# Kernel optimization log

Measured on AMD Instinct MI355X. Metric: run time of the kernel, lower is better.

Reference implementation:

```python
import jax, jax.numpy as jnp
import numpy as np

N, IN, OUT, H = 8192, 128, 64, 4
NEG_SLOPE = 0.2   # GATConv leaky-relu slope
EPS = 1e-5        # BatchNorm1d eps
MASK_VAL = -1e9   # masked_fill value for non-edges (finite for grad safety)


def setup_inputs() -> dict:
    key = jax.random.key(0)
    ks = jax.random.split(key, 5)
    x = jax.random.normal(ks[0], (N, IN), jnp.float32)
    adj = jax.random.randint(ks[1], (N, N), 0, 2, jnp.int32)  # dense 0/1 adjacency
    W = jax.random.normal(ks[2], (H, IN, OUT), jnp.float32) * (1.0 / np.sqrt(IN))
    a_i = jax.random.normal(ks[3], (H, OUT), jnp.float32) * (1.0 / np.sqrt(OUT))
    a_j = jax.random.normal(ks[4], (H, OUT), jnp.float32) * (1.0 / np.sqrt(OUT))
    gamma = jnp.ones((H * OUT,), jnp.float32)   # BN weight
    beta = jnp.zeros((H * OUT,), jnp.float32)   # BN bias
    return {"x": x, "adj": adj, "W": W, "a_i": a_i, "a_j": a_j,
            "gamma": gamma, "beta": beta}


def reference(x, adj, W, a_i, a_j, gamma, beta):
    # --- GATConv (dense adjacency, multi-head, concat) ---
    h = jnp.einsum('ni,hio->hno', x, W)              # [H, N, OUT]
    ei = jnp.einsum('hno,ho->hn', h, a_i)            # [H, N] source scores
    ej = jnp.einsum('hno,ho->hn', h, a_j)            # [H, N] target scores
    coe = ei[:, :, None] + ej[:, None, :]            # [H, N, N]
    coe = jnp.where(coe >= 0, coe, NEG_SLOPE * coe)  # leaky_relu
    coe = jnp.where(adj[None, :, :] == 0, MASK_VAL, coe)
    att = jax.nn.softmax(coe, axis=-1)               # segment softmax over neighbors
    out = jnp.einsum('hnm,hmo->hno', att, h)         # weighted aggregation
    out = jnp.transpose(out, (1, 0, 2)).reshape(N, H * OUT)  # concat heads
    # --- BatchNorm1d (training-mode batch stats over nodes) ---
    mean = jnp.mean(out, axis=0)
    var = jnp.var(out, axis=0)
    out = (out - mean) * jax.lax.rsqrt(var + EPS) * gamma + beta
    # --- ReLU ---
    return jax.nn.relu(out)
```

## Files before the change

kernel.cpp:

```cpp
#include <hip/hip_runtime.h>
#include <hip/hip_bf16.h>

#define NN   8192
#define IND  128
#define OUTD 64
#define NH   4
#define NEG_SLOPE 0.2f
#define BN_EPS 1e-5f

typedef __attribute__((ext_vector_type(8))) short     bf16x8;
typedef __attribute__((ext_vector_type(8))) _Float16  f16x8;
typedef __attribute__((ext_vector_type(2))) _Float16  h2;
typedef __attribute__((ext_vector_type(4))) float     f32x4;
typedef __attribute__((ext_vector_type(4))) int       i32x4;

union V4 { i32x4 i; f16x8 v; };

static __device__ __forceinline__ short f2bf(float f) {
    union { float f; unsigned u; } v; v.f = f;
    return (short)((v.u + 0x8000u) >> 16);
}
static __device__ __forceinline__ unsigned short f2h(float f) {
    union { _Float16 h; unsigned short s; } u; u.h = (_Float16)f; return u.s;
}

__global__ __launch_bounds__(256) void k0_repackW(const float* __restrict__ W,
                                                  short* __restrict__ WB) {
    int tid = blockIdx.x * 256 + threadIdx.x;
    int o = tid & 63, i = (tid >> 6) & 127, h = tid >> 13;
    WB[((h * 16 + (i >> 3)) * 64 + o) * 8 + (i & 7)] = f2bf(W[(h * 128 + i) * 64 + o]);
}

__global__ __launch_bounds__(256) void k1_feat(const float* __restrict__ x,
                                               const short* __restrict__ WB,
                                               const float* __restrict__ a_i,
                                               const float* __restrict__ a_j,
                                               unsigned short* __restrict__ hF,
                                               float* __restrict__ t_Ri,
                                               unsigned short* __restrict__ tE1,
                                               unsigned short* __restrict__ tE2) {
    int w = threadIdx.x >> 6;
    int l = threadIdx.x & 63;
    int quad = l >> 4, lx = l & 15;
    int rb = blockIdx.x;

    f32x4 acc[4] = {};
#pragma unroll
    for (int ks = 0; ks < 4; ++ks) {
        const float* xp = x + (rb * 16 + lx) * IND + ks * 32 + quad * 8;
        f32x4 xa = *(const f32x4*)xp;
        f32x4 xb = *(const f32x4*)(xp + 4);
        bf16x8 af;
#pragma unroll
        for (int j = 0; j < 4; ++j) { af[j] = f2bf(xa[j]); af[4 + j] = f2bf(xb[j]); }
#pragma unroll
        for (int ot = 0; ot < 4; ++ot) {
            bf16x8 bf = *(const bf16x8*)(WB + ((w * 16 + ks * 4 + quad) * 64 + ot * 16 + lx) * 8);
            acc[ot] = __builtin_amdgcn_mfma_f32_16x16x32_bf16(af, bf, acc[ot], 0, 0, 0);
        }
    }
    float aiv[4], ajv[4];
#pragma unroll
    for (int ot = 0; ot < 4; ++ot) {
        aiv[ot] = a_i[w * 64 + ot * 16 + lx];
        ajv[ot] = a_j[w * 64 + ot * 16 + lx];
    }
#pragma unroll
    for (int reg = 0; reg < 4; ++reg) {
        int row = rb * 16 + quad * 4 + reg;
        float ei = 0.f, ej = 0.f;
#pragma unroll
        for (int ot = 0; ot < 4; ++ot) {
            float hv = acc[ot][reg];
            ei += hv * aiv[ot];
            ej += hv * ajv[ot];
        }
#pragma unroll
        for (int m = 1; m <= 8; m <<= 1) {
            ei += __shfl_xor(ei, m, 64);
            ej += __shfl_xor(ej, m, 64);
        }
        if (lx == reg) {
            t_Ri[w * NN + row] = expf(-0.8f * ei);
            tE1[w * NN + row] = f2h(expf(ej));
            tE2[w * NN + row] = f2h(expf(NEG_SLOPE * ej));
        }
#pragma unroll
        for (int ot = 0; ot < 4; ++ot) {
            int o = ot * 16 + lx;
            hF[((w * 1024 + (row >> 3)) * 64 + o) * 8 + (row & 7)] = f2h(acc[ot][reg]);
        }
    }
}

__global__ __launch_bounds__(256) void k2_attn(const int* __restrict__ adj,
                                               const unsigned short* __restrict__ hF,
                                               const float* __restrict__ t_Ri,
                                               const unsigned short* __restrict__ tE1,
                                               const unsigned short* __restrict__ tE2,
                                               float* __restrict__ num,
                                               float* __restrict__ Lsum) {
    __shared__ unsigned char smask[128 * 68];
    __shared__ unsigned int  lutm[256 * 4];
    int tid = threadIdx.x;
    int w = tid >> 6;
    int l = tid & 63;
    int quad = l >> 4, lx = l & 15;
    int rb = blockIdx.x & 127, ks = blockIdx.x >> 7;
    int rowbase = rb * 64;
    int tb = w * NN;
    int k0 = ks * 1024;

    {
        unsigned b = (unsigned)tid;
        i32x4 e;
#pragma unroll
        for (int jj = 0; jj < 4; ++jj) {
            unsigned lo = (b >> (2 * jj)) & 1u, hi = (b >> (2 * jj + 1)) & 1u;
            e[jj] = (int)(lo * 0x3C00u + hi * 0x3C000000u);
        }
        *(i32x4*)&lutm[tid * 4] = e;
    }

    {
        int cg = tid & 127, half = tid >> 7;
        const int* abase = adj + (size_t)rowbase * NN + k0 + cg * 8;
#pragma unroll 2
        for (int rr = 0; rr < 8; ++rr) {
            int rl = half * 8 + rr;
            unsigned mword = 0;
#pragma unroll
            for (int rh = 0; rh < 4; ++rh) {
                const int* ap = abase + (size_t)(rh * 16 + rl) * NN;
                i32x4 a0 = *(const i32x4*)ap;
                i32x4 a1 = *(const i32x4*)(ap + 4);
                unsigned m = 0;
#pragma unroll
                for (int j = 0; j < 4; ++j) {
                    m |= (a0[j] ? 1u : 0u) << j;
                    m |= (a1[j] ? 1u : 0u) << (4 + j);
                }
                mword |= m << (8 * rh);
            }
            *(unsigned int*)&smask[cg * 68 + rl * 4] = mword;
        }
    }
    __syncthreads();

    h2 Rh2[4];
#pragma unroll
    for (int r = 0; r < 4; ++r) {
        _Float16 rv = (_Float16)t_Ri[tb + rowbase + r * 16 + lx];
        Rh2[r][0] = rv; Rh2[r][1] = rv;
    }

    V4 ones;
#pragma unroll
    for (int jj = 0; jj < 4; ++jj) ones.i[jj] = 0x3C003C00;

    f32x4 acc[4][4] = {};
    f32x4 accL[4] = {};

    i32x4 p1, p2;
    V4 pbf[4];
    unsigned pm32;
    {
        int kb = k0 + quad * 8;
        p1 = *(const i32x4*)(tE1 + tb + kb);
        p2 = *(const i32x4*)(tE2 + tb + kb);
#pragma unroll
        for (int ot = 0; ot < 4; ++ot)
            pbf[ot].i = *(const i32x4*)(hF + ((w * 1024 + (kb >> 3)) * 64 + ot * 16 + lx) * 8);
        pm32 = *(const unsigned int*)&smask[quad * 68 + lx * 4];
    }

#pragma unroll 2
    for (int kt = 0; kt < 32; ++kt) {
        i32x4 t1 = p1, t2 = p2;
        unsigned m32 = pm32;
        V4 bfrag[4];
#pragma unroll
        for (int ot = 0; ot < 4; ++ot) bfrag[ot] = pbf[ot];

        int ktn = (kt + 1) & 31;
        int kbn = k0 + ktn * 32 + quad * 8;
        p1 = *(const i32x4*)(tE1 + tb + kbn);
        p2 = *(const i32x4*)(tE2 + tb + kbn);
#pragma unroll
        for (int ot = 0; ot < 4; ++ot)
            pbf[ot].i = *(const i32x4*)(hF + ((w * 1024 + (kbn >> 3)) * 64 + ot * 16 + lx) * 8);
        pm32 = *(const unsigned int*)&smask[(ktn * 4 + quad) * 68 + lx * 4];

        V4 afr[4];
#pragma unroll
        for (int r = 0; r < 4; ++r) {
            V4 mw;
            mw.i = *(const i32x4*)&lutm[((m32 >> (8 * r)) & 0xFFu) * 4];
#pragma unroll
            for (int jj = 0; jj < 4; ++jj) {
                h2 e1 = __builtin_bit_cast(h2, (unsigned)t1[jj]);
                h2 e2 = __builtin_bit_cast(h2, (unsigned)t2[jj]);
                h2 mk = __builtin_bit_cast(h2, (unsigned)mw.i[jj]);
                h2 p  = __builtin_elementwise_max(e1, Rh2[r] * e2) * mk;
                afr[r].i[jj] = (int)__builtin_bit_cast(unsigned, p);
            }
        }
#pragma unroll
        for (int r = 0; r < 4; ++r)
            accL[r] = __builtin_amdgcn_mfma_f32_16x16x32_f16(afr[r].v, ones.v, accL[r], 0, 0, 0);
#pragma unroll
        for (int r = 0; r < 4; ++r)
#pragma unroll
            for (int ot = 0; ot < 4; ++ot)
                acc[r][ot] = __builtin_amdgcn_mfma_f32_16x16x32_f16(afr[r].v, bfrag[ot].v, acc[r][ot], 0, 0, 0);
    }

#pragma unroll
    for (int r = 0; r < 4; ++r)
        if (lx == 0)
#pragma unroll
            for (int reg = 0; reg < 4; ++reg)
                atomicAdd(&Lsum[w * NN + rowbase + r * 16 + quad * 4 + reg], accL[r][reg]);
#pragma unroll
    for (int r = 0; r < 4; ++r)
#pragma unroll
        for (int ot = 0; ot < 4; ++ot)
#pragma unroll
            for (int reg = 0; reg < 4; ++reg) {
                int row = rowbase + r * 16 + quad * 4 + reg;
                atomicAdd(&num[row * 256 + w * 64 + ot * 16 + lx], acc[r][ot][reg]);
            }
}

__global__ __launch_bounds__(256) void k3_stats(const float* __restrict__ num,
                                                const float* __restrict__ Lsum,
                                                float* __restrict__ stats) {
    int c = threadIdx.x;
    int h = c >> 6;
    float s = 0.f, s2 = 0.f;
#pragma unroll
    for (int rr = 0; rr < 8; ++rr) {
        int row = blockIdx.x * 8 + rr;
        float val = num[row * 256 + c] / Lsum[h * NN + row];
        s += val; s2 += val * val;
    }
    atomicAdd(&stats[c], s);
    atomicAdd(&stats[c + 256], s2);
}

__global__ __launch_bounds__(256) void k5_apply(const float* __restrict__ num,
                                                const float* __restrict__ Lsum,
                                                const float* __restrict__ stats,
                                                const float* __restrict__ gamma,
                                                const float* __restrict__ beta,
                                                float* __restrict__ out) {
    __shared__ float sbnp[512];
    int c = threadIdx.x;
    float mean = stats[c] * (1.0f / NN);
    float var  = stats[c + 256] * (1.0f / NN) - mean * mean;
    float sc = gamma[c] * rsqrtf(var + BN_EPS);
    sbnp[c] = sc;
    sbnp[c + 256] = beta[c] - mean * sc;
    __syncthreads();

    int g = blockIdx.x * 256 + threadIdx.x;
    f32x4 v = *(const f32x4*)(num + (size_t)g * 4);
    int cb = (g * 4) & 255;
    int row = g >> 6;
    float rL = 1.0f / Lsum[(cb >> 6) * NN + row];
    f32x4 r;
#pragma unroll
    for (int j = 0; j < 4; ++j)
        r[j] = fmaxf((v[j] * rL) * sbnp[cb + j] + sbnp[256 + cb + j], 0.0f);
    *(f32x4*)(out + (size_t)g * 4) = r;
}

extern "C" void kernel_launch(void* const* d_in, const int* in_sizes, int n_in,
                              void* d_out, int out_size, void* d_ws, size_t ws_size,
                              hipStream_t stream) {
    (void)in_sizes; (void)n_in; (void)out_size; (void)ws_size;
    const float* x     = (const float*)d_in[0];
    const int*   adj   = (const int*)d_in[1];
    const float* W     = (const float*)d_in[2];
    const float* a_i   = (const float*)d_in[3];
    const float* a_j   = (const float*)d_in[4];
    const float* gamma = (const float*)d_in[5];
    const float* beta  = (const float*)d_in[6];
    float* out = (float*)d_out;

    char* ws = (char*)d_ws;
    short*          WB    = (short*)(ws + 0);
    unsigned short* hF    = (unsigned short*)(ws + 65536);
    float*          t_Ri  = (float*)(ws + 4259840);
    unsigned short* tE1   = (unsigned short*)(ws + 4390912);
    unsigned short* tE2   = (unsigned short*)(ws + 4456448);
    float*          num   = (float*)(ws + 4521984);
    float*          Lsum  = (float*)(ws + 12910592);
    float*          stats = (float*)(ws + 13041664);

    (void)hipMemsetAsync(num, 0, 8388608 + 131072 + 2048, stream);

    k0_repackW<<<dim3(128),  dim3(256), 0, stream>>>(W, WB);
    k1_feat   <<<dim3(512),  dim3(256), 0, stream>>>(x, WB, a_i, a_j, hF, t_Ri, tE1, tE2);
    k2_attn   <<<dim3(1024), dim3(256), 0, stream>>>(adj, hF, t_Ri, tE1, tE2, num, Lsum);
    k3_stats  <<<dim3(1024), dim3(256), 0, stream>>>(num, Lsum, stats);
    k5_apply  <<<dim3(2048), dim3(256), 0, stream>>>(num, Lsum, stats, gamma, beta, out);
}
```

Before: 481.7 us.

## Split adjacency bit-packing into a separate kernel and read packed mask from global

Moves the conversion of the dense int32 adjacency into bitmasks out of the attention kernel into a dedicated streaming pack kernel, using nontemporal loads and arithmetic nibble packing that assumes 0/1 values. The attention kernel then loads the precomputed mask words directly from global memory instead of staging them in shared memory. This decouples the bandwidth-bound adjacency read from the compute-heavy attention loop so each can run at its own occupancy. It costs an extra launch and a small global round-trip for the mask, and it relies on adjacency entries being exactly 0 or 1.

Measured after the change: 489.2 us. Within noise of the previous version (+1.6%).

```diff
diff --git a/kernel.cpp b/kernel.cpp
--- a/kernel.cpp
+++ b/kernel.cpp
@@ -29,6 +29,34 @@
     int tid = blockIdx.x * 256 + threadIdx.x;
     int o = tid & 63, i = (tid >> 6) & 127, h = tid >> 13;
     WB[((h * 16 + (i >> 3)) * 64 + o) * 8 + (i & 7)] = f2bf(W[(h * 128 + i) * 64 + o]);
+}
+
+__global__ __launch_bounds__(256) void kC_pack(const int* __restrict__ adj,
+                                               unsigned int* __restrict__ gmask) {
+    int tid = threadIdx.x;
+    int rb = blockIdx.x & 127, ks = blockIdx.x >> 7;
+    int rowbase = rb * 64, k0 = ks * 1024;
+    int cg = tid & 127, half = tid >> 7;
+    const int* abase = adj + (size_t)rowbase * NN + k0 + cg * 8;
+    unsigned wbuf[8];
+#pragma unroll
+    for (int rr = 0; rr < 8; ++rr) {
+        int rl = half * 8 + rr;
+        unsigned mword = 0;
+#pragma unroll
+        for (int rh = 0; rh < 4; ++rh) {
+            const int* ap = abase + (size_t)(rh * 16 + rl) * NN;
+            i32x4 a0 = __builtin_nontemporal_load((const i32x4*)ap);
+            i32x4 a1 = __builtin_nontemporal_load((const i32x4*)(ap + 4));
+            unsigned nib0 = (unsigned)(a0[0] + (a0[1] << 1) + (a0[2] << 2) + (a0[3] << 3));
+            unsigned nib1 = (unsigned)(a1[0] + (a1[1] << 1) + (a1[2] << 2) + (a1[3] << 3));
+            mword |= ((nib1 << 4) | nib0) << (8 * rh);
+        }
+        wbuf[rr] = mword;
+    }
+    unsigned int* dst = gmask + (((size_t)(rb * 8 + ks) * 128 + cg) * 16 + half * 8);
+    *(i32x4*)dst       = *(i32x4*)&wbuf[0];
+    *(i32x4*)(dst + 4) = *(i32x4*)&wbuf[4];
 }
 
 __global__ __launch_bounds__(256) void k1_feat(const float* __restrict__ x,
@@ -93,15 +121,14 @@
     }
 }
 
-__global__ __launch_bounds__(256) void k2_attn(const int* __restrict__ adj,
+__global__ __launch_bounds__(256) void k2_attn(const unsigned int* __restrict__ gmask,
                                                const unsigned short* __restrict__ hF,
                                                const float* __restrict__ t_Ri,
                                                const unsigned short* __restrict__ tE1,
                                                const unsigned short* __restrict__ tE2,
                                                float* __restrict__ num,
                                                float* __restrict__ Lsum) {
-    __shared__ unsigned char smask[128 * 68];
-    __shared__ unsigned int  lutm[256 * 4];
+    __shared__ unsigned int lutm[256 * 4];
     int tid = threadIdx.x;
     int w = tid >> 6;
     int l = tid & 63;
@@ -110,6 +137,7 @@
     int rowbase = rb * 64;
     int tb = w * NN;
     int k0 = ks * 1024;
+    const unsigned int* gm = gmask + (size_t)(rb * 8 + ks) * 128 * 16;
 
     {
         unsigned b = (unsigned)tid;
@@ -120,30 +148,6 @@
             e[jj] = (int)(lo * 0x3C00u + hi * 0x3C000000u);
         }
         *(i32x4*)&lutm[tid * 4] = e;
-    }
-
-    {
-        int cg = tid & 127, half = tid >> 7;
-        const int* abase = adj + (size_t)rowbase * NN + k0 + cg * 8;
-#pragma unroll 2
-        for (int rr = 0; rr < 8; ++rr) {
-            int rl = half * 8 + rr;
-            unsigned mword = 0;
-#pragma unroll
-            for (int rh = 0; rh < 4; ++rh) {
-                const int* ap = abase + (size_t)(rh * 16 + rl) * NN;
-                i32x4 a0 = *(const i32x4*)ap;
-                i32x4 a1 = *(const i32x4*)(ap + 4);
-                unsigned m = 0;
-#pragma unroll
-                for (int j = 0; j < 4; ++j) {
-                    m |= (a0[j] ? 1u : 0u) << j;
-                    m |= (a1[j] ? 1u : 0u) << (4 + j);
-                }
-                mword |= m << (8 * rh);
-            }
-            *(unsigned int*)&smask[cg * 68 + rl * 4] = mword;
-        }
     }
     __syncthreads();
 
@@ -171,7 +175,7 @@
 #pragma unroll
         for (int ot = 0; ot < 4; ++ot)
             pbf[ot].i = *(const i32x4*)(hF + ((w * 1024 + (kb >> 3)) * 64 + ot * 16 + lx) * 8);
-        pm32 = *(const unsigned int*)&smask[quad * 68 + lx * 4];
+        pm32 = gm[quad * 16 + lx];
     }
 
 #pragma unroll 2
@@ -189,7 +193,7 @@
 #pragma unroll
         for (int ot = 0; ot < 4; ++ot)
             pbf[ot].i = *(const i32x4*)(hF + ((w * 1024 + (kbn >> 3)) * 64 + ot * 16 + lx) * 8);
-        pm32 = *(const unsigned int*)&smask[(ktn * 4 + quad) * 68 + lx * 4];
+        pm32 = gm[(ktn * 4 + quad) * 16 + lx];
 
         V4 afr[4];
 #pragma unroll
@@ -297,12 +301,14 @@
     float*          num   = (float*)(ws + 4521984);
     float*          Lsum  = (float*)(ws + 12910592);
     float*          stats = (float*)(ws + 13041664);
+    unsigned int*   gmask = (unsigned int*)(ws + 13043712);
 
     (void)hipMemsetAsync(num, 0, 8388608 + 131072 + 2048, stream);
 
+    kC_pack   <<<dim3(1024), dim3(256), 0, stream>>>(adj, gmask);
     k0_repackW<<<dim3(128),  dim3(256), 0, stream>>>(W, WB);
     k1_feat   <<<dim3(512),  dim3(256), 0, stream>>>(x, WB, a_i, a_j, hF, t_Ri, tE1, tE2);
-    k2_attn   <<<dim3(1024), dim3(256), 0, stream>>>(adj, hF, t_Ri, tE1, tE2, num, Lsum);
+    k2_attn   <<<dim3(1024), dim3(256), 0, stream>>>(gmask, hF, t_Ri, tE1, tE2, num, Lsum);
     k3_stats  <<<dim3(1024), dim3(256), 0, stream>>>(num, Lsum, stats);
     k5_apply  <<<dim3(2048), dim3(256), 0, stream>>>(num, Lsum, stats, gamma, beta, out);
 }
```

## Shrink attention row tile to 16 rows and repack adjacency mask per row

Applied to the files above, without the earlier changes.

The attention kernel now gives each block 16 rows instead of 64, so it launches four times as many blocks and each wave holds a quarter of the accumulators. The adjacency mask is packed with one thread per row and 64-column segment, using arithmetic bit packing that assumes entries are exactly 0 or 1. The aim is more occupancy and parallelism from lower register pressure. The cost is four times as many reads of hF and the exp tables per output row, which raises L2 traffic.

Result: slower. 515.3 us (+7.0%).

```diff
diff --git a/kernel.cpp b/kernel.cpp
--- a/kernel.cpp
+++ b/kernel.cpp
@@ -100,14 +100,14 @@
                                                const unsigned short* __restrict__ tE2,
                                                float* __restrict__ num,
                                                float* __restrict__ Lsum) {
-    __shared__ unsigned char smask[128 * 68];
-    __shared__ unsigned int  lutm[256 * 4];
+    __shared__ unsigned int sw[16 * 34];
+    __shared__ unsigned int lutm[256 * 4];
     int tid = threadIdx.x;
     int w = tid >> 6;
     int l = tid & 63;
     int quad = l >> 4, lx = l & 15;
-    int rb = blockIdx.x & 127, ks = blockIdx.x >> 7;
-    int rowbase = rb * 64;
+    int rt = blockIdx.x & 511, ks = blockIdx.x >> 9;
+    int rowbase = rt * 16;
     int tb = w * NN;
     int k0 = ks * 1024;
 
@@ -123,43 +123,36 @@
     }
 
     {
-        int cg = tid & 127, half = tid >> 7;
-        const int* abase = adj + (size_t)rowbase * NN + k0 + cg * 8;
-#pragma unroll 2
-        for (int rr = 0; rr < 8; ++rr) {
-            int rl = half * 8 + rr;
-            unsigned mword = 0;
-#pragma unroll
-            for (int rh = 0; rh < 4; ++rh) {
-                const int* ap = abase + (size_t)(rh * 16 + rl) * NN;
-                i32x4 a0 = *(const i32x4*)ap;
-                i32x4 a1 = *(const i32x4*)(ap + 4);
-                unsigned m = 0;
-#pragma unroll
-                for (int j = 0; j < 4; ++j) {
-                    m |= (a0[j] ? 1u : 0u) << j;
-                    m |= (a1[j] ? 1u : 0u) << (4 + j);
-                }
-                mword |= m << (8 * rh);
-            }
-            *(unsigned int*)&smask[cg * 68 + rl * 4] = mword;
-        }
+        int row = tid >> 4, s = tid & 15;
+        const int* ap = adj + (size_t)(rowbase + row) * NN + k0 + s * 64;
+        unsigned lo = 0, hi = 0;
+#pragma unroll
+        for (int c = 0; c < 8; ++c) {
+            i32x4 a = *(const i32x4*)(ap + c * 4);
+            lo |= (unsigned)(a[0] + (a[1] << 1) + (a[2] << 2) + (a[3] << 3)) << (4 * c);
+        }
+#pragma unroll
+        for (int c = 8; c < 16; ++c) {
+            i32x4 a = *(const i32x4*)(ap + c * 4);
+            hi |= (unsigned)(a[0] + (a[1] << 1) + (a[2] << 2) + (a[3] << 3)) << (4 * (c - 8));
+        }
+        sw[row * 34 + s * 2]     = lo;
+        sw[row * 34 + s * 2 + 1] = hi;
     }
     __syncthreads();
 
-    h2 Rh2[4];
-#pragma unroll
-    for (int r = 0; r < 4; ++r) {
-        _Float16 rv = (_Float16)t_Ri[tb + rowbase + r * 16 + lx];
-        Rh2[r][0] = rv; Rh2[r][1] = rv;
+    h2 Rh2;
+    {
+        _Float16 rv = (_Float16)t_Ri[tb + rowbase + lx];
+        Rh2[0] = rv; Rh2[1] = rv;
     }
 
     V4 ones;
 #pragma unroll
     for (int jj = 0; jj < 4; ++jj) ones.i[jj] = 0x3C003C00;
 
-    f32x4 acc[4][4] = {};
-    f32x4 accL[4] = {};
+    f32x4 acc[4] = {};
+    f32x4 accL = {};
 
     i32x4 p1, p2;
     V4 pbf[4];
@@ -171,7 +164,7 @@
 #pragma unroll
         for (int ot = 0; ot < 4; ++ot)
             pbf[ot].i = *(const i32x4*)(hF + ((w * 1024 + (kb >> 3)) * 64 + ot * 16 + lx) * 8);
-        pm32 = *(const unsigned int*)&smask[quad * 68 + lx * 4];
+        pm32 = sw[lx * 34 + 0];
     }
 
 #pragma unroll 2
@@ -189,47 +182,35 @@
 #pragma unroll
         for (int ot = 0; ot < 4; ++ot)
             pbf[ot].i = *(const i32x4*)(hF + ((w * 1024 + (kbn >> 3)) * 64 + ot * 16 + lx) * 8);
-        pm32 = *(const unsigned int*)&smask[(ktn * 4 + quad) * 68 + lx * 4];
-
-        V4 afr[4];
-#pragma unroll
-        for (int r = 0; r < 4; ++r) {
-            V4 mw;
-            mw.i = *(const i32x4*)&lutm[((m32 >> (8 * r)) & 0xFFu) * 4];
-#pragma unroll
-            for (int jj = 0; jj < 4; ++jj) {
-                h2 e1 = __builtin_bit_cast(h2, (unsigned)t1[jj]);
-                h2 e2 = __builtin_bit_cast(h2, (unsigned)t2[jj]);
-                h2 mk = __builtin_bit_cast(h2, (unsigned)mw.i[jj]);
-                h2 p  = __builtin_elementwise_max(e1, Rh2[r] * e2) * mk;
-                afr[r].i[jj] = (int)__builtin_bit_cast(unsigned, p);
-            }
-        }
-#pragma unroll
-        for (int r = 0; r < 4; ++r)
-            accL[r] = __builtin_amdgcn_mfma_f32_16x16x32_f16(afr[r].v, ones.v, accL[r], 0, 0, 0);
-#pragma unroll
-        for (int r = 0; r < 4; ++r)
-#pragma unroll
-            for (int ot = 0; ot < 4; ++ot)
-                acc[r][ot] = __builtin_amdgcn_mfma_f32_16x16x32_f16(afr[r].v, bfrag[ot].v, acc[r][ot], 0, 0, 0);
-    }
-
-#pragma unroll
-    for (int r = 0; r < 4; ++r)
-        if (lx == 0)
-#pragma unroll
-            for (int reg = 0; reg < 4; ++reg)
-                atomicAdd(&Lsum[w * NN + rowbase + r * 16 + quad * 4 + reg], accL[r][reg]);
-#pragma unroll
-    for (int r = 0; r < 4; ++r)
+        pm32 = sw[lx * 34 + ktn];
+
+        V4 afr, mw;
+        mw.i = *(const i32x4*)&lutm[((m32 >> (8 * quad)) & 0xFFu) * 4];
+#pragma unroll
+        for (int jj = 0; jj < 4; ++jj) {
+            h2 e1 = __builtin_bit_cast(h2, (unsigned)t1[jj]);
+            h2 e2 = __builtin_bit_cast(h2, (unsigned)t2[jj]);
+            h2 mk = __builtin_bit_cast(h2, (unsigned)mw.i[jj]);
+            h2 p  = __builtin_elementwise_max(e1, Rh2 * e2) * mk;
+            afr.i[jj] = (int)__builtin_bit_cast(unsigned, p);
+        }
+        accL = __builtin_amdgcn_mfma_f32_16x16x32_f16(afr.v, ones.v, accL, 0, 0, 0);
 #pragma unroll
         for (int ot = 0; ot < 4; ++ot)
-#pragma unroll
-            for (int reg = 0; reg < 4; ++reg) {
-                int row = rowbase + r * 16 + quad * 4 + reg;
-                atomicAdd(&num[row * 256 + w * 64 + ot * 16 + lx], acc[r][ot][reg]);
-            }
+            acc[ot] = __builtin_amdgcn_mfma_f32_16x16x32_f16(afr.v, bfrag[ot].v, acc[ot], 0, 0, 0);
+    }
+
+    if (lx == 0)
+#pragma unroll
+        for (int reg = 0; reg < 4; ++reg)
+            atomicAdd(&Lsum[w * NN + rowbase + quad * 4 + reg], accL[reg]);
+#pragma unroll
+    for (int ot = 0; ot < 4; ++ot)
+#pragma unroll
+        for (int reg = 0; reg < 4; ++reg) {
+            int row = rowbase + quad * 4 + reg;
+            atomicAdd(&num[row * 256 + w * 64 + ot * 16 + lx], acc[ot][reg]);
+        }
 }
 
 __global__ __launch_bounds__(256) void k3_stats(const float* __restrict__ num,
@@ -302,7 +283,7 @@
 
     k0_repackW<<<dim3(128),  dim3(256), 0, stream>>>(W, WB);
     k1_feat   <<<dim3(512),  dim3(256), 0, stream>>>(x, WB, a_i, a_j, hF, t_Ri, tE1, tE2);
-    k2_attn   <<<dim3(1024), dim3(256), 0, stream>>>(adj, hF, t_Ri, tE1, tE2, num, Lsum);
+    k2_attn   <<<dim3(4096), dim3(256), 0, stream>>>(adj, hF, t_Ri, tE1, tE2, num, Lsum);
     k3_stats  <<<dim3(1024), dim3(256), 0, stream>>>(num, Lsum, stats);
     k5_apply  <<<dim3(2048), dim3(256), 0, stream>>>(num, Lsum, stats, gamma, beta, out);
 }
```
